# Kernel tuning notes

Hardware: AMD Instinct MI355X
Metric: run time of the kernel (lower is better)

## Reference

```python
import jax, jax.numpy as jnp
import numpy as np

B, L, D, H, FF = 2, 512, 512, 8, 2048
LP1 = L + 1
HD = D // H
RFF_DIM, RB_HID = 32, 64
EPS = 1e-5


def _layernorm(x, g, b):
    mu = jnp.mean(x, axis=-1, keepdims=True)
    var = jnp.mean(jnp.square(x - mu), axis=-1, keepdims=True)
    return (x - mu) * jax.lax.rsqrt(var + EPS) * g + b


def setup_inputs() -> dict:
    key = jax.random.key(0)
    ks = jax.random.split(key, 12)
    def w(k, shape, scale=0.02):
        return jax.random.normal(k, shape, jnp.float32) * scale
    return {
        "x": jax.random.normal(ks[0], (B, LP1, D), jnp.float32),
        "s_norm": jax.random.uniform(ks[1], (B, L), jnp.float32),
        # fixed random-fourier-feature frequencies (requires_grad=False in torch)
        "rff": jax.random.normal(ks[2], (1, RFF_DIM), jnp.float32) * 2.0,
        # rel-bias MLP: Linear(32,64) -> GELU -> Linear(64,nhead), torch (out,in) layout
        "rb_w1": w(ks[3], (RB_HID, RFF_DIM)), "rb_b1": jnp.zeros(RB_HID, jnp.float32),
        "rb_w2": w(ks[4], (H, RB_HID)), "rb_b2": jnp.zeros(H, jnp.float32),
        "n1_g": jnp.ones(D, jnp.float32), "n1_b": jnp.zeros(D, jnp.float32),
        "n2_g": jnp.ones(D, jnp.float32), "n2_b": jnp.zeros(D, jnp.float32),
        # MHA packed qkv in-projection and out-projection
        "in_w": w(ks[5], (3 * D, D)), "in_b": jnp.zeros(3 * D, jnp.float32),
        "out_w": w(ks[6], (D, D)), "out_b": jnp.zeros(D, jnp.float32),
        # FF: Linear(D,FF) -> GELU -> Linear(FF,D)
        "ff_w1": w(ks[7], (FF, D)), "ff_b1": jnp.zeros(FF, jnp.float32),
        "ff_w2": w(ks[8], (D, FF)), "ff_b2": jnp.zeros(D, jnp.float32),
    }


def reference(x, s_norm, rff, rb_w1, rb_b1, rb_w2, rb_b2,
              n1_g, n1_b, n2_g, n2_b, in_w, in_b, out_w, out_b,
              ff_w1, ff_b1, ff_w2, ff_b2):
    b = x.shape[0]
    # s_full: prepend zero for the extra (e.g. CLS) position -> (B, L+1)
    s_full = jnp.concatenate([jnp.zeros((b, 1), x.dtype), s_norm], axis=1)
    # pairwise deltas -> RFF sin features -> 2-layer MLP -> per-head bias
    ds = s_full[:, :, None] - s_full[:, None, :]              # (B, L+1, L+1)
    feat = jnp.sin(ds[..., None] * rff[0])                    # (B, L+1, L+1, 32)
    hid = jax.nn.gelu(feat @ rb_w1.T + rb_b1, approximate=False)
    bias = hid @ rb_w2.T + rb_b2                              # (B, L+1, L+1, H)
    bias = jnp.transpose(bias, (0, 3, 1, 2))                  # (B, H, L+1, L+1)

    # pre-LN self-attention
    z = _layernorm(x, n1_g, n1_b)
    qkv = z @ in_w.T + in_b                                   # (B, L+1, 3D)
    q, k, v = jnp.split(qkv, 3, axis=-1)
    def heads(t):
        return jnp.transpose(t.reshape(b, LP1, H, HD), (0, 2, 1, 3))
    q, k, v = heads(q), heads(k), heads(v)                    # (B, H, L+1, HD)
    scores = jnp.einsum("bhqd,bhkd->bhqk", q, k) / np.sqrt(HD) + bias
    attn = jax.nn.softmax(scores, axis=-1)
    a = jnp.einsum("bhqk,bhkd->bhqd", attn, v)                # (B, H, L+1, HD)
    a = jnp.transpose(a, (0, 2, 1, 3)).reshape(b, LP1, D)
    a = a @ out_w.T + out_b
    x = x + a

    # pre-LN feed-forward
    h2 = _layernorm(x, n2_g, n2_b)
    ffo = jax.nn.gelu(h2 @ ff_w1.T + ff_b1, approximate=False) @ ff_w2.T + ff_b2
    return x + ffo
```

## Files before the change

kernel.cpp:

```cpp
#include <hip/hip_runtime.h>
#include <hip/hip_bf16.h>
#include <math.h>

constexpr int B_   = 2;
constexpr int L_   = 512;
constexpr int LP1  = 513;
constexpr int D_   = 512;
constexpr int H_   = 8;
constexpr int HD_  = 64;
constexpr int FF_  = 2048;
constexpr int RFFD = 32;
constexpr int RBH  = 64;
constexpr int M_   = B_ * LP1;
constexpr float EPS_ = 1e-5f;
constexpr int NT_  = 8193;
constexpr int QB_  = 2;
constexpr int QBLKS_ = (LP1 + QB_ - 1) / QB_;

constexpr size_t OFFZ   = 0;
constexpr size_t OFFX1  = OFFZ  + (size_t)M_ * D_;
constexpr size_t OFFQKV = OFFX1 + (size_t)M_ * D_;
constexpr size_t OFFKT  = OFFQKV + (size_t)M_ * 3 * D_;
constexpr size_t OFFA   = OFFKT + (size_t)B_ * D_ * LP1;
constexpr size_t OFFT   = OFFA + (size_t)M_ * D_;

typedef __attribute__((ext_vector_type(4))) float f32x4;
typedef __attribute__((ext_vector_type(8))) __bf16 bf16x8;
typedef __attribute__((ext_vector_type(4))) __bf16 bf16x4;

__device__ __forceinline__ float gelu_exact(float x) {
    return 0.5f * x * (1.0f + erff(x * 0.70710678118654752f));
}

__device__ __forceinline__ __bf16 f2b(float f) {
    union { float f; unsigned u; } a; a.f = f;
    const unsigned r = (a.u + 0x7FFFu + ((a.u >> 16) & 1u)) >> 16;
    union { unsigned short s; __bf16 b; } o; o.s = (unsigned short)r;
    return o.b;
}

__global__ void k_btab(const float* __restrict__ rff, const float* __restrict__ w1,
                       const float* __restrict__ b1, const float* __restrict__ w2,
                       const float* __restrict__ b2, float* __restrict__ table) {
    const int idx = blockIdx.x * 256 + threadIdx.x;
    if (idx >= NT_) return;
    const float ds = (float)idx * (2.0f / (NT_ - 1)) - 1.0f;
    float feat[RFFD];
    #pragma unroll
    for (int k = 0; k < RFFD; ++k) feat[k] = sinf(ds * rff[k]);
    float bh[H_];
    #pragma unroll
    for (int h = 0; h < H_; ++h) bh[h] = b2[h];
    for (int l = 0; l < RBH; ++l) {
        float acc = b1[l];
        #pragma unroll
        for (int k = 0; k < RFFD; ++k) acc += feat[k] * w1[l * RFFD + k];
        const float gl = gelu_exact(acc);
        #pragma unroll
        for (int h = 0; h < H_; ++h) bh[h] += gl * w2[h * RBH + l];
    }
    #pragma unroll
    for (int h = 0; h < H_; ++h) table[(size_t)idx * H_ + h] = bh[h];
}

__global__ void k_ln(const float* __restrict__ x, const float* __restrict__ g,
                     const float* __restrict__ be, float* __restrict__ out) {
    const int m = blockIdx.x;
    const int t = threadIdx.x;
    __shared__ float red[256];
    const float v0 = x[(size_t)m * D_ + t];
    const float v1 = x[(size_t)m * D_ + t + 256];
    red[t] = v0 + v1;
    __syncthreads();
    for (int off = 128; off > 0; off >>= 1) {
        if (t < off) red[t] += red[t + off];
        __syncthreads();
    }
    const float mu = red[0] * (1.0f / D_);
    __syncthreads();
    const float d0 = v0 - mu, d1 = v1 - mu;
    red[t] = d0 * d0 + d1 * d1;
    __syncthreads();
    for (int off = 128; off > 0; off >>= 1) {
        if (t < off) red[t] += red[t + off];
        __syncthreads();
    }
    const float rstd = rsqrtf(red[0] * (1.0f / D_) + EPS_);
    out[(size_t)m * D_ + t]       = d0 * rstd * g[t]       + be[t];
    out[(size_t)m * D_ + t + 256] = d1 * rstd * g[t + 256] + be[t + 256];
}

template <int ACT, bool RES>
__global__ __launch_bounds__(256)
void k_gemm_mfma(const float* __restrict__ A, const float* __restrict__ W,
                 const float* __restrict__ bias, const float* __restrict__ res,
                 float* __restrict__ C, int M, int N, int K) {
    constexpr int BM = 64, BN = 64, BK = 32, PAD = 8;
    __shared__ __bf16 As[BM][BK + PAD];
    __shared__ __bf16 Bs[BN][BK + PAD];
    const int t    = threadIdx.x;
    const int m0   = blockIdx.y * BM;
    const int n0   = blockIdx.x * BN;
    const int wid  = t >> 6;
    const int lane = t & 63;
    const int wr   = (wid >> 1) * 32;
    const int wc   = (wid & 1) * 32;
    const int fr   = lane & 15;
    const int kg   = lane >> 4;

    f32x4 acc[2][2] = {};

    for (int k0 = 0; k0 < K; k0 += BK) {
        #pragma unroll
        for (int i = 0; i < 2; ++i) {
            const int idx = t + i * 256;
            const int row = idx >> 3;
            const int f4  = idx & 7;
            float4 av = make_float4(0.f, 0.f, 0.f, 0.f);
            const int gm = m0 + row;
            if (gm < M) av = *(const float4*)&A[(size_t)gm * K + k0 + f4 * 4];
            bf16x4 ab;
            ab[0] = f2b(av.x); ab[1] = f2b(av.y); ab[2] = f2b(av.z); ab[3] = f2b(av.w);
            *(bf16x4*)&As[row][f4 * 4] = ab;
            const float4 wv = *(const float4*)&W[(size_t)(n0 + row) * K + k0 + f4 * 4];
            bf16x4 wb;
            wb[0] = f2b(wv.x); wb[1] = f2b(wv.y); wb[2] = f2b(wv.z); wb[3] = f2b(wv.w);
            *(bf16x4*)&Bs[row][f4 * 4] = wb;
        }
        __syncthreads();
        const bf16x8 af0 = *(const bf16x8*)&As[wr + fr][kg * 8];
        const bf16x8 af1 = *(const bf16x8*)&As[wr + 16 + fr][kg * 8];
        const bf16x8 bf0 = *(const bf16x8*)&Bs[wc + fr][kg * 8];
        const bf16x8 bf1 = *(const bf16x8*)&Bs[wc + 16 + fr][kg * 8];
        acc[0][0] = __builtin_amdgcn_mfma_f32_16x16x32_bf16(af0, bf0, acc[0][0], 0, 0, 0);
        acc[0][1] = __builtin_amdgcn_mfma_f32_16x16x32_bf16(af0, bf1, acc[0][1], 0, 0, 0);
        acc[1][0] = __builtin_amdgcn_mfma_f32_16x16x32_bf16(af1, bf0, acc[1][0], 0, 0, 0);
        acc[1][1] = __builtin_amdgcn_mfma_f32_16x16x32_bf16(af1, bf1, acc[1][1], 0, 0, 0);
        __syncthreads();
    }

    #pragma unroll
    for (int ti = 0; ti < 2; ++ti) {
        #pragma unroll
        for (int tj = 0; tj < 2; ++tj) {
            const int gn = n0 + wc + tj * 16 + fr;
            const float bv = bias[gn];
            #pragma unroll
            for (int v = 0; v < 4; ++v) {
                const int gm = m0 + wr + ti * 16 + kg * 4 + v;
                if (gm < M) {
                    float val = acc[ti][tj][v] + bv;
                    if (ACT == 1) val = gelu_exact(val);
                    if (RES) val += res[(size_t)gm * N + gn];
                    C[(size_t)gm * N + gn] = val;
                }
            }
        }
    }
}

__global__ void k_kT(const float* __restrict__ qkv, float* __restrict__ kT) {
    __shared__ float tile[32][33];
    const int b  = blockIdx.z;
    const int j0 = blockIdx.x * 32;
    const int d0 = blockIdx.y * 32;
    const int tx = threadIdx.x;
    const int ty = threadIdx.y;
    #pragma unroll
    for (int q = 0; q < 4; ++q) {
        const int j = j0 + ty + q * 8;
        if (j < LP1)
            tile[ty + q * 8][tx] = qkv[((size_t)(b * LP1 + j)) * (3 * D_) + D_ + d0 + tx];
    }
    __syncthreads();
    #pragma unroll
    for (int q = 0; q < 4; ++q) {
        const int j = j0 + tx;
        const int d = d0 + ty + q * 8;
        if (j < LP1)
            kT[((size_t)b * D_ + d) * LP1 + j] = tile[tx][ty + q * 8];
    }
}

__global__ __launch_bounds__(256)
void k_attn(const float* __restrict__ qkv, const float* __restrict__ kT,
            const float* __restrict__ s_norm, const float* __restrict__ table,
            float* __restrict__ a) {
    const int b   = blockIdx.x / QBLKS_;
    const int qi0 = (blockIdx.x % QBLKS_) * QB_;
    const int t = threadIdx.x;
    __shared__ float q_s[QB_][D_];
    __shared__ float s_s[LP1 + 1];
    __shared__ float p_s[QB_][H_][LP1 + 3];

    for (int idx = t; idx < QB_ * D_; idx += 256) {
        const int q = idx >> 9;
        const int d = idx & 511;
        const int i = min(qi0 + q, LP1 - 1);
        q_s[q][d] = qkv[(size_t)(b * LP1 + i) * (3 * D_) + d];
    }
    for (int j = t; j < LP1; j += 256)
        s_s[j] = (j == 0) ? 0.f : s_norm[b * L_ + j - 1];
    __syncthreads();

    const int g  = t >> 5;
    const int sl = t & 31;
    constexpr int NJ = 17;

    float s_i[QB_];
    #pragma unroll
    for (int q = 0; q < QB_; ++q) s_i[q] = s_s[min(qi0 + q, LP1 - 1)];

    float acc[QB_][NJ] = {};
    const float* kTg = kT + ((size_t)b * D_ + g * HD_) * LP1;
    for (int dd = 0; dd < HD_; ++dd) {
        const float* row = kTg + (size_t)dd * LP1;
        float qv[QB_];
        #pragma unroll
        for (int q = 0; q < QB_; ++q) qv[q] = q_s[q][g * HD_ + dd];
        #pragma unroll
        for (int jj = 0; jj < NJ; ++jj) {
            const int j = sl + jj * 32;
            const float kv = (j < LP1) ? row[j] : 0.f;
            #pragma unroll
            for (int q = 0; q < QB_; ++q) acc[q][jj] = fmaf(qv[q], kv, acc[q][jj]);
        }
    }

    #pragma unroll
    for (int q = 0; q < QB_; ++q) {
        float mx = -1e30f;
        #pragma unroll
        for (int jj = 0; jj < NJ; ++jj) {
            const int j = sl + jj * 32;
            if (j < LP1) {
                const float ds = s_i[q] - s_s[j];
                float u = (ds + 1.0f) * ((NT_ - 1) * 0.5f);
                u = fminf(fmaxf(u, 0.0f), (float)(NT_ - 2));
                const int i0 = (int)u;
                const float f = u - (float)i0;
                const float b0  = table[(size_t)i0 * H_ + g];
                const float b1v = table[(size_t)(i0 + 1) * H_ + g];
                acc[q][jj] = b0 + f * (b1v - b0) + 0.125f * acc[q][jj];
                mx = fmaxf(mx, acc[q][jj]);
            }
        }
        #pragma unroll
        for (int off = 16; off > 0; off >>= 1) mx = fmaxf(mx, __shfl_xor(mx, off, 32));
        float sum = 0.f;
        #pragma unroll
        for (int jj = 0; jj < NJ; ++jj) {
            const int j = sl + jj * 32;
            if (j < LP1) {
                acc[q][jj] = __expf(acc[q][jj] - mx);
                sum += acc[q][jj];
            }
        }
        #pragma unroll
        for (int off = 16; off > 0; off >>= 1) sum += __shfl_xor(sum, off, 32);
        const float inv = 1.0f / sum;
        #pragma unroll
        for (int jj = 0; jj < NJ; ++jj) {
            const int j = sl + jj * 32;
            if (j < LP1) p_s[q][g][j] = acc[q][jj] * inv;
        }
    }
    __syncthreads();

    const float* vbase = qkv + (size_t)(b * LP1) * (3 * D_) + 2 * D_;
    for (int e = t; e < D_; e += 256) {
        const int h = e >> 6;
        float o00 = 0.f, o01 = 0.f, o10 = 0.f, o11 = 0.f;
        int j = 0;
        for (; j + 2 <= LP1; j += 2) {
            const float v0 = vbase[(size_t)(j + 0) * (3 * D_) + e];
            const float v1 = vbase[(size_t)(j + 1) * (3 * D_) + e];
            o00 = fmaf(p_s[0][h][j + 0], v0, o00);
            o01 = fmaf(p_s[0][h][j + 1], v1, o01);
            o10 = fmaf(p_s[1][h][j + 0], v0, o10);
            o11 = fmaf(p_s[1][h][j + 1], v1, o11);
        }
        for (; j < LP1; ++j) {
            const float v0 = vbase[(size_t)j * (3 * D_) + e];
            o00 = fmaf(p_s[0][h][j], v0, o00);
            o10 = fmaf(p_s[1][h][j], v0, o10);
        }
        if (qi0 < LP1)
            a[(size_t)(b * LP1 + qi0) * D_ + e] = o00 + o01;
        if (qi0 + 1 < LP1)
            a[(size_t)(b * LP1 + qi0 + 1) * D_ + e] = o10 + o11;
    }
}

extern "C" void kernel_launch(void* const* d_in, const int* in_sizes, int n_in,
                              void* d_out, int out_size, void* d_ws, size_t ws_size,
                              hipStream_t stream) {
    const float* x      = (const float*)d_in[0];
    const float* s_norm = (const float*)d_in[1];
    const float* rff    = (const float*)d_in[2];
    const float* rb_w1  = (const float*)d_in[3];
    const float* rb_b1  = (const float*)d_in[4];
    const float* rb_w2  = (const float*)d_in[5];
    const float* rb_b2  = (const float*)d_in[6];
    const float* n1_g   = (const float*)d_in[7];
    const float* n1_b   = (const float*)d_in[8];
    const float* n2_g   = (const float*)d_in[9];
    const float* n2_b   = (const float*)d_in[10];
    const float* in_w   = (const float*)d_in[11];
    const float* in_b   = (const float*)d_in[12];
    const float* out_w  = (const float*)d_in[13];
    const float* out_b  = (const float*)d_in[14];
    const float* ff_w1  = (const float*)d_in[15];
    const float* ff_b1  = (const float*)d_in[16];
    const float* ff_w2  = (const float*)d_in[17];
    const float* ff_b2  = (const float*)d_in[18];

    float* ws    = (float*)d_ws;
    float* z     = ws + OFFZ;
    float* x1    = ws + OFFX1;
    float* qkv   = ws + OFFQKV;
    float* kT    = ws + OFFKT;
    float* a     = ws + OFFA;
    float* table = ws + OFFT;
    float* h2    = z;
    float* hact  = qkv;

    k_btab<<<(NT_ + 255) / 256, 256, 0, stream>>>(rff, rb_w1, rb_b1, rb_w2, rb_b2, table);
    k_ln<<<M_, 256, 0, stream>>>(x, n1_g, n1_b, z);
    k_gemm_mfma<0, false><<<dim3(3 * D_ / 64, (M_ + 63) / 64), 256, 0, stream>>>(
        z, in_w, in_b, nullptr, qkv, M_, 3 * D_, D_);
    k_kT<<<dim3((LP1 + 31) / 32, D_ / 32, B_), dim3(32, 8), 0, stream>>>(qkv, kT);
    k_attn<<<B_ * QBLKS_, 256, 0, stream>>>(qkv, kT, s_norm, table, a);
    k_gemm_mfma<0, true><<<dim3(D_ / 64, (M_ + 63) / 64), 256, 0, stream>>>(
        a, out_w, out_b, x, x1, M_, D_, D_);
    k_ln<<<M_, 256, 0, stream>>>(x1, n2_g, n2_b, h2);
    k_gemm_mfma<1, false><<<dim3(FF_ / 64, (M_ + 63) / 64), 256, 0, stream>>>(
        h2, ff_w1, ff_b1, nullptr, hact, M_, FF_, D_);
    k_gemm_mfma<0, true><<<dim3(D_ / 64, (M_ + 63) / 64), 256, 0, stream>>>(
        hact, ff_w2, ff_b2, x1, (float*)d_out, M_, D_, FF_);
}
```

Before: 339.0 us.

## Double-buffer GEMM tiles, add XCD-aware block remap, use BM=32 for narrow GEMMs

Restructures the MFMA GEMM so the next K tile is prefetched into registers while the current one is computed, storing it into a second LDS buffer. This leaves one barrier per iteration instead of two and hides global load latency. It also flattens the grid and remaps block IDs so neighbouring tiles land on the same XCD for better L2 reuse. The N=512 GEMMs use a 32-row M tile to launch more blocks. The cost is higher register and LDS use per block, plus smaller per-wave MFMA work in the BM=32 variant.

```diff
diff --git a/kernel.cpp b/kernel.cpp
--- a/kernel.cpp
+++ b/kernel.cpp
@@ -90,59 +90,100 @@
     out[(size_t)m * D_ + t + 256] = d1 * rstd * g[t + 256] + be[t + 256];
 }
 
-template <int ACT, bool RES>
+template <int ACT, bool RES, int BM>
 __global__ __launch_bounds__(256)
 void k_gemm_mfma(const float* __restrict__ A, const float* __restrict__ W,
                  const float* __restrict__ bias, const float* __restrict__ res,
                  float* __restrict__ C, int M, int N, int K) {
-    constexpr int BM = 64, BN = 64, BK = 32, PAD = 8;
-    __shared__ __bf16 As[BM][BK + PAD];
-    __shared__ __bf16 Bs[BN][BK + PAD];
-    const int t    = threadIdx.x;
-    const int m0   = blockIdx.y * BM;
-    const int n0   = blockIdx.x * BN;
+    constexpr int BN = 64, BK = 32, PAD = 8;
+    constexpr int LA = (BM * BK) / (4 * 256);
+    constexpr int WRT = 2;
+    constexpr int WCT = (BM == 64) ? 2 : 1;
+    __shared__ __bf16 As[2][BM][BK + PAD];
+    __shared__ __bf16 Bs[2][BN][BK + PAD];
+    const int t = threadIdx.x;
+
+    const int nx = N / BN;
+    int bid = blockIdx.x;
+    {
+        const int nb = gridDim.x;
+        const int q = nb >> 3, r = nb & 7;
+        const int xc = bid & 7, o = bid >> 3;
+        bid = (xc < r ? xc * (q + 1) : r * (q + 1) + (xc - r) * q) + o;
+    }
+    const int m0 = (bid / nx) * BM;
+    const int n0 = (bid % nx) * BN;
+
     const int wid  = t >> 6;
     const int lane = t & 63;
-    const int wr   = (wid >> 1) * 32;
-    const int wc   = (wid & 1) * 32;
+    const int wr   = (BM == 64) ? ((wid >> 1) * 32) : 0;
+    const int wc   = (BM == 64) ? ((wid & 1) * 32) : (wid * 16);
     const int fr   = lane & 15;
     const int kg   = lane >> 4;
-
-    f32x4 acc[2][2] = {};
-
-    for (int k0 = 0; k0 < K; k0 += BK) {
+    const int lrow = t >> 3;
+    const int lf4  = t & 7;
+
+    f32x4 acc[WRT][WCT] = {};
+    float4 pa[LA], pw[2];
+    const int nk = K / BK;
+
+    auto load_tile = [&](int kt) {
+        const int kbase = kt * BK + lf4 * 4;
+        #pragma unroll
+        for (int i = 0; i < LA; ++i) {
+            const int gm = m0 + lrow + i * 32;
+            pa[i] = make_float4(0.f, 0.f, 0.f, 0.f);
+            if (gm < M) pa[i] = *(const float4*)&A[(size_t)gm * K + kbase];
+        }
+        #pragma unroll
+        for (int i = 0; i < 2; ++i)
+            pw[i] = *(const float4*)&W[(size_t)(n0 + lrow + i * 32) * K + kbase];
+    };
+    auto store_tile = [&](int buf) {
+        #pragma unroll
+        for (int i = 0; i < LA; ++i) {
+            bf16x4 v;
+            v[0] = f2b(pa[i].x); v[1] = f2b(pa[i].y);
+            v[2] = f2b(pa[i].z); v[3] = f2b(pa[i].w);
+            *(bf16x4*)&As[buf][lrow + i * 32][lf4 * 4] = v;
+        }
         #pragma unroll
         for (int i = 0; i < 2; ++i) {
-            const int idx = t + i * 256;
-            const int row = idx >> 3;
-            const int f4  = idx & 7;
-            float4 av = make_float4(0.f, 0.f, 0.f, 0.f);
-            const int gm = m0 + row;
-            if (gm < M) av = *(const float4*)&A[(size_t)gm * K + k0 + f4 * 4];
-            bf16x4 ab;
-            ab[0] = f2b(av.x); ab[1] = f2b(av.y); ab[2] = f2b(av.z); ab[3] = f2b(av.w);
-            *(bf16x4*)&As[row][f4 * 4] = ab;
-            const float4 wv = *(const float4*)&W[(size_t)(n0 + row) * K + k0 + f4 * 4];
-            bf16x4 wb;
-            wb[0] = f2b(wv.x); wb[1] = f2b(wv.y); wb[2] = f2b(wv.z); wb[3] = f2b(wv.w);
-            *(bf16x4*)&Bs[row][f4 * 4] = wb;
-        }
+            bf16x4 v;
+            v[0] = f2b(pw[i].x); v[1] = f2b(pw[i].y);
+            v[2] = f2b(pw[i].z); v[3] = f2b(pw[i].w);
+            *(bf16x4*)&Bs[buf][lrow + i * 32][lf4 * 4] = v;
+        }
+    };
+
+    load_tile(0);
+    store_tile(0);
+    __syncthreads();
+    int cur = 0;
+    for (int kt = 0; kt < nk; ++kt) {
+        if (kt + 1 < nk) load_tile(kt + 1);
+        bf16x8 af[WRT], bfr[WCT];
+        #pragma unroll
+        for (int i2 = 0; i2 < WRT; ++i2)
+            af[i2] = *(const bf16x8*)&As[cur][wr + i2 * 16 + fr][kg * 8];
+        #pragma unroll
+        for (int j2 = 0; j2 < WCT; ++j2)
+            bfr[j2] = *(const bf16x8*)&Bs[cur][wc + j2 * 16 + fr][kg * 8];
+        #pragma unroll
+        for (int i2 = 0; i2 < WRT; ++i2)
+            #pragma unroll
+            for (int j2 = 0; j2 < WCT; ++j2)
+                acc[i2][j2] = __builtin_amdgcn_mfma_f32_16x16x32_bf16(
+                    af[i2], bfr[j2], acc[i2][j2], 0, 0, 0);
+        if (kt + 1 < nk) store_tile(cur ^ 1);
         __syncthreads();
-        const bf16x8 af0 = *(const bf16x8*)&As[wr + fr][kg * 8];
-        const bf16x8 af1 = *(const bf16x8*)&As[wr + 16 + fr][kg * 8];
-        const bf16x8 bf0 = *(const bf16x8*)&Bs[wc + fr][kg * 8];
-        const bf16x8 bf1 = *(const bf16x8*)&Bs[wc + 16 + fr][kg * 8];
-        acc[0][0] = __builtin_amdgcn_mfma_f32_16x16x32_bf16(af0, bf0, acc[0][0], 0, 0, 0);
-        acc[0][1] = __builtin_amdgcn_mfma_f32_16x16x32_bf16(af0, bf1, acc[0][1], 0, 0, 0);
-        acc[1][0] = __builtin_amdgcn_mfma_f32_16x16x32_bf16(af1, bf0, acc[1][0], 0, 0, 0);
-        acc[1][1] = __builtin_amdgcn_mfma_f32_16x16x32_bf16(af1, bf1, acc[1][1], 0, 0, 0);
-        __syncthreads();
-    }
-
-    #pragma unroll
-    for (int ti = 0; ti < 2; ++ti) {
-        #pragma unroll
-        for (int tj = 0; tj < 2; ++tj) {
+        cur ^= 1;
+    }
+
+    #pragma unroll
+    for (int ti = 0; ti < WRT; ++ti) {
+        #pragma unroll
+        for (int tj = 0; tj < WCT; ++tj) {
             const int gn = n0 + wc + tj * 16 + fr;
             const float bv = bias[gn];
             #pragma unroll
@@ -327,15 +368,15 @@
 
     k_btab<<<(NT_ + 255) / 256, 256, 0, stream>>>(rff, rb_w1, rb_b1, rb_w2, rb_b2, table);
     k_ln<<<M_, 256, 0, stream>>>(x, n1_g, n1_b, z);
-    k_gemm_mfma<0, false><<<dim3(3 * D_ / 64, (M_ + 63) / 64), 256, 0, stream>>>(
+    k_gemm_mfma<0, false, 64><<<(3 * D_ / 64) * ((M_ + 63) / 64), 256, 0, stream>>>(
         z, in_w, in_b, nullptr, qkv, M_, 3 * D_, D_);
     k_kT<<<dim3((LP1 + 31) / 32, D_ / 32, B_), dim3(32, 8), 0, stream>>>(qkv, kT);
     k_attn<<<B_ * QBLKS_, 256, 0, stream>>>(qkv, kT, s_norm, table, a);
-    k_gemm_mfma<0, true><<<dim3(D_ / 64, (M_ + 63) / 64), 256, 0, stream>>>(
+    k_gemm_mfma<0, true, 32><<<(D_ / 64) * ((M_ + 31) / 32), 256, 0, stream>>>(
         a, out_w, out_b, x, x1, M_, D_, D_);
     k_ln<<<M_, 256, 0, stream>>>(x1, n2_g, n2_b, h2);
-    k_gemm_mfma<1, false><<<dim3(FF_ / 64, (M_ + 63) / 64), 256, 0, stream>>>(
+    k_gemm_mfma<1, false, 64><<<(FF_ / 64) * ((M_ + 63) / 64), 256, 0, stream>>>(
         h2, ff_w1, ff_b1, nullptr, hact, M_, FF_, D_);
-    k_gemm_mfma<0, true><<<dim3(D_ / 64, (M_ + 63) / 64), 256, 0, stream>>>(
+    k_gemm_mfma<0, true, 32><<<(D_ / 64) * ((M_ + 31) / 32), 256, 0, stream>>>(
         hact, ff_w2, ff_b2, x1, (float*)d_out, M_, D_, FF_);
 }
```

Result: faster. 299.2 us (-11.7%).
